# Performance work log

Measured on AMD Instinct MI355X. Metric: run time of the kernel, lower is better.

The kernel has to match this reference:

```python
import jax, jax.numpy as jnp
import numpy as np

NBITS = 4
QMAX = 2 ** (NBITS - 1) - 1   # 7
QMIN = -(2 ** (NBITS - 1))    # -8


def quantize_weight(W):
    # Brevitas-style symmetric per-tensor int4 weight quantization with STE.
    scale = jnp.max(jnp.abs(W)) / QMAX
    q = jnp.clip(jnp.round(W / scale), QMIN, QMAX) * scale
    # straight-through estimator (no-op for fwd-only, kept for parity)
    return W + jax.lax.stop_gradient(q - W)


def setup_inputs() -> dict:
    key = jax.random.key(0)
    k1, k2, k3 = jax.random.split(key, 3)
    x = jax.random.normal(k1, (8192, 4, 16, 16, 16), dtype=jnp.float32)
    W = jax.random.normal(k2, (4, 2048), dtype=jnp.float32) * 0.02
    b = jax.random.normal(k3, (4,), dtype=jnp.float32) * 0.01
    return {"x": x, "W": W, "b": b}


def reference(x, W, b):
    B, C, D, H, Wd = x.shape
    # MaxPool3d(kernel=2, stride=2): reshape-and-reduce (dims are divisible by 2)
    pooled = x.reshape(B, C, D // 2, 2, H // 2, 2, Wd // 2, 2).max(axis=(3, 5, 7))
    flat = pooled.reshape(B, -1)                      # [B, 2048]
    Wq = quantize_weight(W)                           # int4-dequantized weight
    logits = jnp.einsum("bf,of->bo", flat, Wq) + b    # [B, 4]
    return jax.nn.softmax(logits, axis=1)
```

## Files before the change

### kernel.cpp

```cpp
#include <hip/hip_runtime.h>
#include <hip/hip_bf16.h>
#include <math.h>

__global__ void quant_w_kernel(const float* __restrict__ W,
                               float* __restrict__ wqt ) {
    __shared__ float smax[4];
    const int t = threadIdx.x;
    float m = 0.0f;
    for (int i = t; i < 4 * 2048; i += 256) m = fmaxf(m, fabsf(W[i]));
    #pragma unroll
    for (int off = 32; off; off >>= 1) m = fmaxf(m, __shfl_down(m, off));
    if ((t & 63) == 0) smax[t >> 6] = m;
    __syncthreads();
    const float M = fmaxf(fmaxf(smax[0], smax[1]), fmaxf(smax[2], smax[3]));
    const float scale = M / 7.0f;
    for (int i = t; i < 4 * 2048; i += 256) {
        float w = W[i];
        float q = rintf(w / scale);
        q = fminf(fmaxf(q, -8.0f), 7.0f);
        const int o = i >> 11;
        const int f = i & 2047;
        wqt[f * 4 + o] = q * scale;
    }
}

__global__ __launch_bounds__(256) void fused_pool_linear_softmax(
        const float* __restrict__ x,
        const float* __restrict__ wqt,
        const float* __restrict__ bias,
        float* __restrict__ out) {
    const int b = blockIdx.x;
    const float* __restrict__ xb = x + (size_t)b * 16384;
    const int t = threadIdx.x;

    float4 acc = make_float4(0.f, 0.f, 0.f, 0.f);

    #pragma unroll
    for (int it = 0; it < 4; ++it) {
        const int G  = t + 256 * it;
        const int q  = G & 3;
        const int hp = (G >> 2) & 7;
        const int dp = (G >> 5) & 7;
        const int c  = G >> 8;
        const int base = c * 4096 + (dp << 1) * 256 + (hp << 1) * 16 + (q << 2);

        const float4 v00 = *(const float4*)(xb + base);
        const float4 v01 = *(const float4*)(xb + base + 16);
        const float4 v10 = *(const float4*)(xb + base + 256);
        const float4 v11 = *(const float4*)(xb + base + 272);

        const float p0 = fmaxf(fmaxf(fmaxf(v00.x, v00.y), fmaxf(v01.x, v01.y)),
                               fmaxf(fmaxf(v10.x, v10.y), fmaxf(v11.x, v11.y)));
        const float p1 = fmaxf(fmaxf(fmaxf(v00.z, v00.w), fmaxf(v01.z, v01.w)),
                               fmaxf(fmaxf(v10.z, v10.w), fmaxf(v11.z, v11.w)));

        const int f0 = c * 512 + dp * 64 + hp * 8 + (q << 1);
        const float4 w0 = *(const float4*)(wqt + f0 * 4);
        const float4 w1 = *(const float4*)(wqt + (f0 + 1) * 4);

        acc.x += p0 * w0.x + p1 * w1.x;
        acc.y += p0 * w0.y + p1 * w1.y;
        acc.z += p0 * w0.z + p1 * w1.z;
        acc.w += p0 * w0.w + p1 * w1.w;
    }

    #pragma unroll
    for (int off = 32; off; off >>= 1) {
        acc.x += __shfl_down(acc.x, off);
        acc.y += __shfl_down(acc.y, off);
        acc.z += __shfl_down(acc.z, off);
        acc.w += __shfl_down(acc.w, off);
    }

    __shared__ float4 red[4];
    const int wave = t >> 6;
    if ((t & 63) == 0) red[wave] = acc;
    __syncthreads();

    if (t == 0) {
        float l0 = red[0].x + red[1].x + red[2].x + red[3].x + bias[0];
        float l1 = red[0].y + red[1].y + red[2].y + red[3].y + bias[1];
        float l2 = red[0].z + red[1].z + red[2].z + red[3].z + bias[2];
        float l3 = red[0].w + red[1].w + red[2].w + red[3].w + bias[3];
        const float m  = fmaxf(fmaxf(l0, l1), fmaxf(l2, l3));
        const float e0 = expf(l0 - m), e1 = expf(l1 - m),
                    e2 = expf(l2 - m), e3 = expf(l3 - m);
        const float inv = 1.0f / (e0 + e1 + e2 + e3);
        *(float4*)(out + (size_t)b * 4) =
            make_float4(e0 * inv, e1 * inv, e2 * inv, e3 * inv);
    }
}

extern "C" void kernel_launch(void* const* d_in, const int* in_sizes, int n_in,
                              void* d_out, int out_size, void* d_ws, size_t ws_size,
                              hipStream_t stream) {
    const float* x    = (const float*)d_in[0];
    const float* W    = (const float*)d_in[1];
    const float* bias = (const float*)d_in[2];
    float* out = (float*)d_out;
    float* wqt = (float*)d_ws;

    quant_w_kernel<<<1, 256, 0, stream>>>(W, wqt);
    fused_pool_linear_softmax<<<8192, 256, 0, stream>>>(x, wqt, bias, out);
}
```

Baseline: 681.5 us.

## Assign one wave per batch row with contiguous loads and shuffle-based pooling

The main kernel now gives each wavefront one batch row, four rows per block, so the cross-wave shared-memory reduction and block barrier go away. Each lane streams contiguous float4 rows and finishes the 2x2x2 max-pool with a lane-xor shuffle instead of gathering strided rows, which is meant to improve coalescing and reduce per-block overhead on a memory-bound pass. The weight quantization kernel is widened to 1024 threads that each load two float4s and reduce once. The cost is extra shuffles and a select per iteration, plus larger per-wave serial loops.

```diff
diff --git a/kernel.cpp b/kernel.cpp
--- a/kernel.cpp
+++ b/kernel.cpp
@@ -1,27 +1,45 @@
 #include <hip/hip_runtime.h>
-#include <hip/hip_bf16.h>
 #include <math.h>
 
-__global__ void quant_w_kernel(const float* __restrict__ W,
-                               float* __restrict__ wqt ) {
-    __shared__ float smax[4];
+__global__ __launch_bounds__(1024) void quant_w_kernel(
+        const float* __restrict__ W, float* __restrict__ wqt ) {
+    __shared__ float smax[16];
+    __shared__ float sscale;
     const int t = threadIdx.x;
-    float m = 0.0f;
-    for (int i = t; i < 4 * 2048; i += 256) m = fmaxf(m, fabsf(W[i]));
+    const float4 v0 = ((const float4*)W)[t];
+    const float4 v1 = ((const float4*)W)[t + 1024];
+
+    float m = fmaxf(
+        fmaxf(fmaxf(fabsf(v0.x), fabsf(v0.y)), fmaxf(fabsf(v0.z), fabsf(v0.w))),
+        fmaxf(fmaxf(fabsf(v1.x), fabsf(v1.y)), fmaxf(fabsf(v1.z), fabsf(v1.w))));
     #pragma unroll
-    for (int off = 32; off; off >>= 1) m = fmaxf(m, __shfl_down(m, off));
+    for (int off = 32; off; off >>= 1) m = fmaxf(m, __shfl_xor(m, off));
     if ((t & 63) == 0) smax[t >> 6] = m;
     __syncthreads();
-    const float M = fmaxf(fmaxf(smax[0], smax[1]), fmaxf(smax[2], smax[3]));
-    const float scale = M / 7.0f;
-    for (int i = t; i < 4 * 2048; i += 256) {
-        float w = W[i];
-        float q = rintf(w / scale);
-        q = fminf(fmaxf(q, -8.0f), 7.0f);
-        const int o = i >> 11;
-        const int f = i & 2047;
-        wqt[f * 4 + o] = q * scale;
+    if (t == 0) {
+        float M = smax[0];
+        #pragma unroll
+        for (int i = 1; i < 16; ++i) M = fmaxf(M, smax[i]);
+        sscale = M / 7.0f;
     }
+    __syncthreads();
+    const float scale = sscale;
+
+#define QSTORE(val, idx)                                              \
+    {                                                                 \
+        const int i_ = (idx);                                         \
+        const int o_ = i_ >> 11;             \
+        const int f_ = i_ & 2047;                        \
+        float q_ = rintf((val) / scale);    \
+        q_ = fminf(fmaxf(q_, -8.0f), 7.0f);                           \
+        wqt[f_ * 4 + o_] = q_ * scale;                                \
+    }
+    const int i0 = t << 2;
+    QSTORE(v0.x, i0 + 0); QSTORE(v0.y, i0 + 1);
+    QSTORE(v0.z, i0 + 2); QSTORE(v0.w, i0 + 3);
+    QSTORE(v1.x, i0 + 4096); QSTORE(v1.y, i0 + 4097);
+    QSTORE(v1.z, i0 + 4098); QSTORE(v1.w, i0 + 4099);
+#undef QSTORE
 }
 
 __global__ __launch_bounds__(256) void fused_pool_linear_softmax(
@@ -29,59 +47,61 @@
         const float* __restrict__ wqt,
         const float* __restrict__ bias,
         float* __restrict__ out) {
-    const int b = blockIdx.x;
-    const float* __restrict__ xb = x + (size_t)b * 16384;
-    const int t = threadIdx.x;
+    const int t  = threadIdx.x;
+    const int wv = t >> 6;
+    const int l  = t & 63;
+    const int b  = (blockIdx.x << 2) + wv;
+
+    const float* __restrict__ p = x + (size_t)b * 16384 + (l << 2);
+    const int hodd = (l >> 2) & 1;
+    const int f0   = hodd * 64 + (l >> 3) * 8 + ((l & 3) << 1);
+    const float* __restrict__ wp = wqt + f0 * 4;
 
     float4 acc = make_float4(0.f, 0.f, 0.f, 0.f);
 
-    #pragma unroll
-    for (int it = 0; it < 4; ++it) {
-        const int G  = t + 256 * it;
-        const int q  = G & 3;
-        const int hp = (G >> 2) & 7;
-        const int dp = (G >> 5) & 7;
-        const int c  = G >> 8;
-        const int base = c * 4096 + (dp << 1) * 256 + (hp << 1) * 16 + (q << 2);
+    #pragma unroll 4
+    for (int it = 0; it < 16; ++it) {
+        const float4 v0 = *(const float4*)(p);
+        const float4 v1 = *(const float4*)(p + 256);
+        const float4 v2 = *(const float4*)(p + 512);
+        const float4 v3 = *(const float4*)(p + 768);
+        p += 1024;
 
-        const float4 v00 = *(const float4*)(xb + base);
-        const float4 v01 = *(const float4*)(xb + base + 16);
-        const float4 v10 = *(const float4*)(xb + base + 256);
-        const float4 v11 = *(const float4*)(xb + base + 272);
+        const float aA = fmaxf(fmaxf(v0.x, v0.y), fmaxf(v1.x, v1.y));
+        const float bA = fmaxf(fmaxf(v0.z, v0.w), fmaxf(v1.z, v1.w));
+        const float aB = fmaxf(fmaxf(v2.x, v2.y), fmaxf(v3.x, v3.y));
+        const float bB = fmaxf(fmaxf(v2.z, v2.w), fmaxf(v3.z, v3.w));
 
-        const float p0 = fmaxf(fmaxf(fmaxf(v00.x, v00.y), fmaxf(v01.x, v01.y)),
-                               fmaxf(fmaxf(v10.x, v10.y), fmaxf(v11.x, v11.y)));
-        const float p1 = fmaxf(fmaxf(fmaxf(v00.z, v00.w), fmaxf(v01.z, v01.w)),
-                               fmaxf(fmaxf(v10.z, v10.w), fmaxf(v11.z, v11.w)));
+        const float saA = __shfl_xor(aA, 4);
+        const float sbA = __shfl_xor(bA, 4);
+        const float saB = __shfl_xor(aB, 4);
+        const float sbB = __shfl_xor(bB, 4);
 
-        const int f0 = c * 512 + dp * 64 + hp * 8 + (q << 1);
-        const float4 w0 = *(const float4*)(wqt + f0 * 4);
-        const float4 w1 = *(const float4*)(wqt + (f0 + 1) * 4);
+        const float p0 = hodd ? fmaxf(aB, saB) : fmaxf(aA, saA);
+        const float p1 = hodd ? fmaxf(bB, sbB) : fmaxf(bA, sbA);
 
-        acc.x += p0 * w0.x + p1 * w1.x;
-        acc.y += p0 * w0.y + p1 * w1.y;
-        acc.z += p0 * w0.z + p1 * w1.z;
-        acc.w += p0 * w0.w + p1 * w1.w;
+        const float4 w0 = *(const float4*)(wp);
+        const float4 w1 = *(const float4*)(wp + 4);
+        wp += 512;
+
+        acc.x = fmaf(p0, w0.x, fmaf(p1, w1.x, acc.x));
+        acc.y = fmaf(p0, w0.y, fmaf(p1, w1.y, acc.y));
+        acc.z = fmaf(p0, w0.z, fmaf(p1, w1.z, acc.z));
+        acc.w = fmaf(p0, w0.w, fmaf(p1, w1.w, acc.w));
     }
 
     #pragma unroll
     for (int off = 32; off; off >>= 1) {
-        acc.x += __shfl_down(acc.x, off);
-        acc.y += __shfl_down(acc.y, off);
-        acc.z += __shfl_down(acc.z, off);
-        acc.w += __shfl_down(acc.w, off);
+        acc.x += __shfl_xor(acc.x, off);
+        acc.y += __shfl_xor(acc.y, off);
+        acc.z += __shfl_xor(acc.z, off);
+        acc.w += __shfl_xor(acc.w, off);
     }
 
-    __shared__ float4 red[4];
-    const int wave = t >> 6;
-    if ((t & 63) == 0) red[wave] = acc;
-    __syncthreads();
-
-    if (t == 0) {
-        float l0 = red[0].x + red[1].x + red[2].x + red[3].x + bias[0];
-        float l1 = red[0].y + red[1].y + red[2].y + red[3].y + bias[1];
-        float l2 = red[0].z + red[1].z + red[2].z + red[3].z + bias[2];
-        float l3 = red[0].w + red[1].w + red[2].w + red[3].w + bias[3];
+    if (l == 0) {
+        const float4 bi = *(const float4*)bias;
+        const float l0 = acc.x + bi.x, l1 = acc.y + bi.y,
+                    l2 = acc.z + bi.z, l3 = acc.w + bi.w;
         const float m  = fmaxf(fmaxf(l0, l1), fmaxf(l2, l3));
         const float e0 = expf(l0 - m), e1 = expf(l1 - m),
                     e2 = expf(l2 - m), e3 = expf(l3 - m);
@@ -100,6 +120,6 @@
     float* out = (float*)d_out;
     float* wqt = (float*)d_ws;
 
-    quant_w_kernel<<<1, 256, 0, stream>>>(W, wqt);
-    fused_pool_linear_softmax<<<8192, 256, 0, stream>>>(x, wqt, bias, out);
+    quant_w_kernel<<<1, 1024, 0, stream>>>(W, wqt);
+    fused_pool_linear_softmax<<<2048, 256, 0, stream>>>(x, wqt, bias, out);
 }
```

Result: no change. 682.6 us (+0.2%).
